# Kernel optimization log

Measured on AMD Instinct MI355X. Metric: run time of the kernel, lower is better.

The kernel has to match this reference:

```python
import jax, jax.numpy as jnp
import numpy as np
from jax import lax

H = 8          # num_heads
STATE = 16     # SSM state_dim
EPS = 1e-5


def layer_norm(x, g, b):
    mu = jnp.mean(x, axis=-1, keepdims=True)
    var = jnp.mean((x - mu) ** 2, axis=-1, keepdims=True)
    return (x - mu) / jnp.sqrt(var + EPS) * g + b


def linear(x, w, b):
    # torch nn.Linear convention: w [out,in]
    return x @ w.T + b


def cross_attn(q_in, kv_in, qw, qb, kw, kb, vw, vb, ow, ob, g, beta):
    B, Lq, D = q_in.shape
    Lk = kv_in.shape[1]
    hd = D // H
    Q = linear(q_in, qw, qb).reshape(B, Lq, H, hd).transpose(0, 2, 1, 3)
    K = linear(kv_in, kw, kb).reshape(B, Lk, H, hd).transpose(0, 2, 1, 3)
    V = linear(kv_in, vw, vb).reshape(B, Lk, H, hd).transpose(0, 2, 1, 3)
    scores = jnp.einsum('bhqd,bhkd->bhqk', Q, K) / (hd ** 0.5)
    w = jax.nn.softmax(scores, axis=-1)
    out = jnp.einsum('bhqk,bhkd->bhqd', w, V)
    out = out.transpose(0, 2, 1, 3).reshape(B, Lq, D)
    out = linear(out, ow, ob)
    out = layer_norm(out + q_in, g, beta)
    return out, w


def ssm(x, in_w, in_b, A, Bm, C, gw, gb, ow, ob):
    B, L, D = x.shape
    xp = linear(x, in_w, in_b)                      # [B,L,2D]
    x_in = xp[..., D:]                              # second chunk
    gate = jax.nn.sigmoid(linear(x, gw, gb))
    x_in = x_in * gate
    def step(h, xt):
        h = h @ A.T + xt @ Bm.T                     # [B,STATE]
        return h, h @ C.T                           # y [B,D]
    h0 = jnp.zeros((B, STATE), dtype=x.dtype)
    _, ys = lax.scan(step, h0, x_in.transpose(1, 0, 2))
    ys = ys.transpose(1, 0, 2)
    return linear(ys, ow, ob)


def mamba_block(x, p, i):
    y = ssm(layer_norm(x, p['m_ln1_g'][i], p['m_ln1_b'][i]),
            p['m_in_w'][i], p['m_in_b'][i], p['m_A'][i], p['m_B'][i], p['m_C'][i],
            p['m_gate_w'][i], p['m_gate_b'][i], p['m_sout_w'][i], p['m_sout_b'][i])
    x = x + y
    h = layer_norm(x, p['m_ln2_g'][i], p['m_ln2_b'][i])
    h = linear(h, p['m_f1_w'][i], p['m_f1_b'][i])
    h = jax.nn.gelu(h, approximate=False)
    h = linear(h, p['m_f2_w'][i], p['m_f2_b'][i])
    return x + h


def setup_inputs() -> dict:
    key = jax.random.key(0)
    ks = iter(jax.random.split(key, 64))
    B, L, D, BD, VD = 1024, 32, 256, 128, 256
    nB = 6
    def rn(shape, s=0.02):
        return jax.random.normal(next(ks), shape, dtype=jnp.float32) * s
    inp = {
        'ble_features': jax.random.normal(next(ks), (B, L, BD), dtype=jnp.float32),
        'visual_features': jax.random.normal(next(ks), (B, L, VD), dtype=jnp.float32),
        # modality projections
        'bp_w': rn((D, BD)), 'bp_b': jnp.zeros(D), 'bp_emb': rn((D,)),
        'bp_g': jnp.ones(D), 'bp_beta': jnp.zeros(D),
        'vp_w': rn((D, VD)), 'vp_b': jnp.zeros(D), 'vp_emb': rn((D,)),
        'vp_g': jnp.ones(D), 'vp_beta': jnp.zeros(D),
        # two cross-attentions stacked on axis 0: [0]=ble->vis, [1]=vis->ble
        'a_qw': rn((2, D, D)), 'a_qb': jnp.zeros((2, D)),
        'a_kw': rn((2, D, D)), 'a_kb': jnp.zeros((2, D)),
        'a_vw': rn((2, D, D)), 'a_vb': jnp.zeros((2, D)),
        'a_ow': rn((2, D, D)), 'a_ob': jnp.zeros((2, D)),
        'a_g': jnp.ones((2, D)), 'a_beta': jnp.zeros((2, D)),
        # 6 mamba blocks stacked on axis 0
        'm_ln1_g': jnp.ones((nB, D)), 'm_ln1_b': jnp.zeros((nB, D)),
        'm_in_w': rn((nB, 2 * D, D)), 'm_in_b': jnp.zeros((nB, 2 * D)),
        'm_A': rn((nB, STATE, STATE)), 'm_B': rn((nB, STATE, D)), 'm_C': rn((nB, D, STATE)),
        'm_gate_w': rn((nB, D, D)), 'm_gate_b': jnp.zeros((nB, D)),
        'm_sout_w': rn((nB, D, D)), 'm_sout_b': jnp.zeros((nB, D)),
        'm_ln2_g': jnp.ones((nB, D)), 'm_ln2_b': jnp.zeros((nB, D)),
        'm_f1_w': rn((nB, 4 * D, D)), 'm_f1_b': jnp.zeros((nB, 4 * D)),
        'm_f2_w': rn((nB, D, 4 * D)), 'm_f2_b': jnp.zeros((nB, D)),
        # final projection
        'fin_g': jnp.ones(D), 'fin_beta': jnp.zeros(D),
        'fin_w': rn((D, D)), 'fin_b': jnp.zeros(D),
    }
    return inp


def reference(ble_features, visual_features,
              bp_w, bp_b, bp_emb, bp_g, bp_beta,
              vp_w, vp_b, vp_emb, vp_g, vp_beta,
              a_qw, a_qb, a_kw, a_kb, a_vw, a_vb, a_ow, a_ob, a_g, a_beta,
              m_ln1_g, m_ln1_b, m_in_w, m_in_b, m_A, m_B, m_C,
              m_gate_w, m_gate_b, m_sout_w, m_sout_b,
              m_ln2_g, m_ln2_b, m_f1_w, m_f1_b, m_f2_w, m_f2_b,
              fin_g, fin_beta, fin_w, fin_b):
    ble = layer_norm(linear(ble_features, bp_w, bp_b) + bp_emb, bp_g, bp_beta)
    vis = layer_norm(linear(visual_features, vp_w, vp_b) + vp_emb, vp_g, vp_beta)
    # seq_len == target_length -> align_sequences is identity
    ble_att, w_b2v = cross_attn(ble, vis, a_qw[0], a_qb[0], a_kw[0], a_kb[0],
                                a_vw[0], a_vb[0], a_ow[0], a_ob[0], a_g[0], a_beta[0])
    vis_att, w_v2b = cross_attn(vis, ble, a_qw[1], a_qb[1], a_kw[1], a_kb[1],
                                a_vw[1], a_vb[1], a_ow[1], a_ob[1], a_g[1], a_beta[1])
    fused = ble_att + vis_att
    p = dict(m_ln1_g=m_ln1_g, m_ln1_b=m_ln1_b, m_in_w=m_in_w, m_in_b=m_in_b,
             m_A=m_A, m_B=m_B, m_C=m_C, m_gate_w=m_gate_w, m_gate_b=m_gate_b,
             m_sout_w=m_sout_w, m_sout_b=m_sout_b, m_ln2_g=m_ln2_g, m_ln2_b=m_ln2_b,
             m_f1_w=m_f1_w, m_f1_b=m_f1_b, m_f2_w=m_f2_w, m_f2_b=m_f2_b)
    for i in range(m_A.shape[0]):
        fused = mamba_block(fused, p, i)
    g = jnp.mean(fused, axis=1)
    g = layer_norm(g, fin_g, fin_beta)
    g = jax.nn.gelu(linear(g, fin_w, fin_b), approximate=False)
    wb = jnp.mean(w_b2v, axis=(1, 2, 3))
    wv = jnp.mean(w_v2b, axis=(1, 2, 3))
    tot = wb + wv + 1e-6
    return (g, wb / tot, wv / tot)
```

## Files before the change

### kernel.cpp

```cpp
#include <hip/hip_runtime.h>
#include <hip/hip_bf16.h>
#include <math.h>

static constexpr int Bsz  = 1024;
static constexpr int Lseq = 32;
static constexpr int Dm   = 256;
static constexpr int NROW = Bsz * Lseq;

typedef __attribute__((ext_vector_type(8))) short bf16x8;
typedef __attribute__((ext_vector_type(4))) float f32x4;

__device__ __forceinline__ float sigm_f(float x) {
    return 1.0f / (1.0f + __expf(-x));
}
__device__ __forceinline__ float gelu_f(float x) {
    const float u = x * (0.7978845608028654f + 0.0356774081f * x * x);
    return x * sigm_f(2.0f * u);
}
__device__ __forceinline__ float b2f(ushort u) {
    union { float f; uint v; } t; t.v = ((uint)u) << 16; return t.f;
}
__device__ __forceinline__ ushort f2b(float f) {
    union { float f; uint v; } t; t.f = f;
    const uint lsb = (t.v >> 16) & 1u;
    t.v += 0x7fffu + lsb;
    return (ushort)(t.v >> 16);
}

#define GLDS(gp, lp) __builtin_amdgcn_global_load_lds( \
    (const __attribute__((address_space(1))) void*)(gp), \
    (__attribute__((address_space(3))) void*)(lp), 16, 0, 0)


template<int ACT, bool OUTBF, int OMAP, int DUAL>
__global__ __launch_bounds__(256)
void mgemm(const ushort* __restrict__ X, const ushort* __restrict__ W,
           const ushort* __restrict__ W2,
           const float* __restrict__ b1, const float* __restrict__ b2,
           float* __restrict__ Cf, ushort* __restrict__ Cb,
           ushort* __restrict__ Cb2, int K, int M)
{
    __shared__ ushort As[8192];
    __shared__ ushort Bs[8192];
    __shared__ ushort Bs2[DUAL ? 8192 : 8];
    const int tid = threadIdx.x;
    const int w = tid >> 6, l = tid & 63;

    int f = blockIdx.y * gridDim.x + blockIdx.x;
    const int nwg = gridDim.x * gridDim.y;
    if ((nwg & 7) == 0) f = (f & 7) * (nwg >> 3) + (f >> 3);
    const int n0 = (f / gridDim.x) << 7;
    const int m0 = (f % gridDim.x) << 7;

    const int ric = l >> 3;
    const int sl  = l & 7;
    const ushort* gAp[4]; const ushort* gBp[4]; const ushort* gCp[DUAL ? 4 : 1];
    ushort* lAp[4]; ushort* lBp[4]; ushort* lCp[DUAL ? 4 : 1];
    #pragma unroll
    for (int c = 0; c < 4; ++c) {
        const int r = ((w << 2) + c) * 8 + ric;
        const int eo = (sl ^ (r & 7)) << 3;
        gAp[c] = X + (size_t)(n0 + r) * K + eo;
        gBp[c] = W + (size_t)(m0 + r) * K + eo;
        lAp[c] = As + (((w << 2) + c) << 9) ;
        lBp[c] = Bs + (((w << 2) + c) << 9);
        if constexpr (DUAL) {
            gCp[c] = W2 + (size_t)(m0 + r) * K + eo;
            lCp[c] = Bs2 + (((w << 2) + c) << 9);
        }
    }

    const int wr = (w >> 1) & 1, wc = w & 1;
    const int cl = l & 15, kg = l >> 4;
    int aoff[2][4], boff[2][4];
    #pragma unroll
    for (int sub = 0; sub < 2; ++sub) {
        const int s = sub * 4 + kg;
        #pragma unroll
        for (int m = 0; m < 4; ++m) {
            const int r = wr * 64 + m * 16 + cl;
            aoff[sub][m] = r * 64 + ((s ^ (r & 7)) << 3);
        }
        #pragma unroll
        for (int n = 0; n < 4; ++n) {
            const int r = wc * 64 + n * 16 + cl;
            boff[sub][n] = r * 64 + ((s ^ (r & 7)) << 3);
        }
    }

    f32x4 acc[4][4];
    f32x4 acc2[DUAL ? 4 : 1][DUAL ? 4 : 1];
    #pragma unroll
    for (int m = 0; m < 4; ++m)
        #pragma unroll
        for (int n = 0; n < 4; ++n) {
            acc[m][n] = (f32x4){0.f, 0.f, 0.f, 0.f};
            if constexpr (DUAL) acc2[m][n] = (f32x4){0.f, 0.f, 0.f, 0.f};
        }

    for (int kc = 0; kc < K; kc += 64) {
        #pragma unroll
        for (int c = 0; c < 4; ++c) {
            GLDS(gAp[c], lAp[c]); gAp[c] += 64;
            GLDS(gBp[c], lBp[c]); gBp[c] += 64;
            if constexpr (DUAL) { GLDS(gCp[c], lCp[c]); gCp[c] += 64; }
        }
        __syncthreads();
        #pragma unroll
        for (int sub = 0; sub < 2; ++sub) {
            bf16x8 av[4], bv[4];
            #pragma unroll
            for (int m = 0; m < 4; ++m) av[m] = *(const bf16x8*)(As + aoff[sub][m]);
            #pragma unroll
            for (int n = 0; n < 4; ++n) bv[n] = *(const bf16x8*)(Bs + boff[sub][n]);
            #pragma unroll
            for (int m = 0; m < 4; ++m)
                #pragma unroll
                for (int n = 0; n < 4; ++n)
                    acc[m][n] = __builtin_amdgcn_mfma_f32_16x16x32_bf16(
                        av[m], bv[n], acc[m][n], 0, 0, 0);
            if constexpr (DUAL) {
                bf16x8 cv[4];
                #pragma unroll
                for (int n = 0; n < 4; ++n) cv[n] = *(const bf16x8*)(Bs2 + boff[sub][n]);
                #pragma unroll
                for (int m = 0; m < 4; ++m)
                    #pragma unroll
                    for (int n = 0; n < 4; ++n)
                        acc2[m][n] = __builtin_amdgcn_mfma_f32_16x16x32_bf16(
                            av[m], cv[n], acc2[m][n], 0, 0, 0);
            }
        }
        __syncthreads();
    }

    const int colb = m0 + wc * 64 + cl;
    const int rowb = n0 + wr * 64 + (kg << 2);
    float biasA[4], biasB[4];
    #pragma unroll
    for (int n = 0; n < 4; ++n) {
        biasA[n] = (b1 != nullptr) ? b1[colb + n * 16] : 0.0f;
        if constexpr (DUAL) biasB[n] = b2[colb + n * 16];
    }

    if constexpr (OUTBF || DUAL != 0) {
        ushort* Rw = (w == 0) ? As : (w == 1) ? As + 4096
                   : (w == 2) ? Bs : Bs + 4096;
        const int rr = l >> 3, rc8 = (l & 7) << 3;
        const int nout = (DUAL == 2) ? 2 : 1;
        for (int which = 0; which < nout; ++which) {
            #pragma unroll
            for (int m = 0; m < 4; ++m)
                #pragma unroll
                for (int j = 0; j < 4; ++j) {
                    const int lrow = m * 16 + (kg << 2) + j;
                    #pragma unroll
                    for (int n = 0; n < 4; ++n) {
                        float v;
                        if (which == 0) {
                            v = acc[m][n][j] + biasA[n];
                            if constexpr (DUAL == 1)
                                v = sigm_f(v) * (acc2[m][n][j] + biasB[n]);
                            else if (ACT == 1) v = sigm_f(v);
                            else if (ACT == 2) v = gelu_f(v);
                        } else {
                            v = acc2[m][n][j] + biasB[n];
                        }
                        const int lcol = (n << 4) + cl;
                        Rw[lrow * 64 + (lcol ^ (((lrow >> 1) & 7) << 3))] = f2b(v);
                    }
                }
            ushort* dst = (which == 0) ? Cb : Cb2;
            #pragma unroll
            for (int p = 0; p < 8; ++p) {
                const int lrow = (p << 3) + rr;
                const bf16x8 v8 = *(const bf16x8*)(
                    Rw + lrow * 64 + (rc8 ^ (((lrow >> 1) & 7) << 3)));
                const size_t grow = (size_t)(n0 + wr * 64 + lrow);
                const int gcol = m0 + wc * 64 + rc8;
                size_t idx;
                if (OMAP == 1) idx = grow * 2048 + ((size_t)(gcol >> 4) << 6) + (gcol & 15);
                else           idx = grow * (size_t)M + gcol;
                *(bf16x8*)(dst + idx) = v8;
            }
        }
    } else {
        #pragma unroll
        for (int m = 0; m < 4; ++m)
            #pragma unroll
            for (int j = 0; j < 4; ++j) {
                const size_t row = (size_t)(rowb + m * 16 + j);
                #pragma unroll
                for (int n = 0; n < 4; ++n) {
                    float v = acc[m][n][j] + biasA[n];
                    if (ACT == 1) v = sigm_f(v);
                    else if (ACT == 2) v = gelu_f(v);
                    Cf[row * (size_t)M + colb + n * 16] = v;
                }
            }
    }
}

template<bool ADD_E, bool ACC_F, bool WRV, int LNOUT, bool HASB2>
__global__ __launch_bounds__(256)
void growln_k(const ushort* __restrict__ X, const ushort* __restrict__ W,
              const float* __restrict__ b1, const float* __restrict__ b2,
              const float* __restrict__ E, const float* __restrict__ g,
              const float* __restrict__ bt, float* __restrict__ Fres,
              ushort* __restrict__ Yb, int K)
{
    __shared__ ushort As[32 * 64];
    __shared__ ushort Bs[256 * 64];
    __shared__ float sred[32][2];
    __shared__ float qred[32][2];
    const int tid = threadIdx.x;
    const int w = tid >> 6, l = tid & 63;
    const int n0 = blockIdx.x << 5;
    const int rowg = w >> 1, colg = w & 1;

    const int ric = l >> 3, sl = l & 7;
    const ushort* gB[8]; ushort* lB[8];
    #pragma unroll
    for (int c = 0; c < 8; ++c) {
        const int rB = ((w << 3) + c) * 8 + ric;
        gB[c] = W + (size_t)rB * K + ((sl ^ (rB & 7)) << 3);
        lB[c] = Bs + (((w << 3) + c) << 9);
    }
    const int rA = (w << 3) + ric;
    const ushort* gA = X + (size_t)(n0 + rA) * K + ((sl ^ (rA & 7)) << 3);
    ushort* lA = As + (w << 9);

    const int cl = l & 15, kg = l >> 4;
    const int ar = rowg * 16 + cl;
    int aoff[2], boff[2][8];
    #pragma unroll
    for (int sub = 0; sub < 2; ++sub) {
        const int s = sub * 4 + kg;
        aoff[sub] = ar * 64 + ((s ^ (ar & 7)) << 3);
        #pragma unroll
        for (int n = 0; n < 8; ++n) {
            const int br = colg * 128 + n * 16 + cl;
            boff[sub][n] = br * 64 + ((s ^ (br & 7)) << 3);
        }
    }

    f32x4 acc[8];
    #pragma unroll
    for (int n = 0; n < 8; ++n) acc[n] = (f32x4){0.f, 0.f, 0.f, 0.f};

    for (int kc = 0; kc < K; kc += 64) {
        #pragma unroll
        for (int c = 0; c < 8; ++c) { GLDS(gB[c], lB[c]); gB[c] += 64; }
        GLDS(gA, lA); gA += 64;
        __syncthreads();
        #pragma unroll
        for (int sub = 0; sub < 2; ++sub) {
            const bf16x8 av = *(const bf16x8*)(As + aoff[sub]);
            #pragma unroll
            for (int n = 0; n < 8; ++n) {
                const bf16x8 bv = *(const bf16x8*)(Bs + boff[sub][n]);
                acc[n] = __builtin_amdgcn_mfma_f32_16x16x32_bf16(av, bv, acc[n], 0, 0, 0);
            }
        }
        __syncthreads();
    }

    float bA[8];
    #pragma unroll
    for (int n = 0; n < 8; ++n) {
        const int col = colg * 128 + n * 16 + cl;
        float v = (b1 != nullptr) ? b1[col] : 0.0f;
        if (HASB2) v += b2[col];
        bA[n] = v;
    }
    float gg[8], bb[8];
    if (LNOUT > 0) {
        #pragma unroll
        for (int n = 0; n < 8; ++n) {
            const int col = colg * 128 + n * 16 + cl;
            gg[n] = g[col]; bb[n] = bt[col];
        }
    }

    #pragma unroll
    for (int j = 0; j < 4; ++j) {
        const int lrow = rowg * 16 + (kg << 2) + j;
        const size_t rb = (size_t)(n0 + lrow) << 8;
        float s = 0.0f;
        #pragma unroll
        for (int n = 0; n < 8; ++n) {
            const size_t idx = rb + colg * 128 + n * 16 + cl;
            float x = acc[n][j] + bA[n];
            if (ADD_E) x += E[idx];
            if (ACC_F) x += Fres[idx];
            acc[n][j] = x; s += x;
        }
        if (WRV) {
            #pragma unroll
            for (int n = 0; n < 8; ++n)
                Fres[rb + colg * 128 + n * 16 + cl] = acc[n][j];
        }
        if (LNOUT > 0) {
            #pragma unroll
            for (int o = 1; o < 16; o <<= 1) s += __shfl_xor(s, o);
            if (cl == 0) sred[lrow][colg] = s;
        }
    }
    if (LNOUT > 0) {
        __syncthreads();
        float mu[4];
        #pragma unroll
        for (int j = 0; j < 4; ++j) {
            const int lrow = rowg * 16 + (kg << 2) + j;
            mu[j] = (sred[lrow][0] + sred[lrow][1]) * (1.0f / 256.0f);
            float q = 0.0f;
            #pragma unroll
            for (int n = 0; n < 8; ++n) { const float d = acc[n][j] - mu[j]; q += d * d; }
            #pragma unroll
            for (int o = 1; o < 16; o <<= 1) q += __shfl_xor(q, o);
            if (cl == 0) qred[lrow][colg] = q;
        }
        __syncthreads();
        #pragma unroll
        for (int j = 0; j < 4; ++j) {
            const int lrow = rowg * 16 + (kg << 2) + j;
            const size_t rb = (size_t)(n0 + lrow) << 8;
            const float rstd = rsqrtf((qred[lrow][0] + qred[lrow][1]) * (1.0f / 256.0f) + 1e-5f);
            #pragma unroll
            for (int n = 0; n < 8; ++n) {
                const float y = (acc[n][j] - mu[j]) * rstd * gg[n] + bb[n];
                const size_t idx = rb + colg * 128 + n * 16 + cl;
                if (LNOUT & 1) Yb[idx] = f2b(y);
                if (LNOUT == 2 || LNOUT == 3) Fres[idx] = y;
                if (LNOUT == 4) Fres[idx] += y;
            }
        }
    }
}

__global__ __launch_bounds__(256)
void ln_k(const float* __restrict__ X, const float* __restrict__ g,
          const float* __restrict__ bt, ushort* __restrict__ Yb)
{
    const int lane = threadIdx.x & 63;
    const int row  = (blockIdx.x << 2) + (threadIdx.x >> 6);
    const size_t base = (size_t)row * Dm + (lane << 2);
    float4 v = *reinterpret_cast<const float4*>(&X[base]);
    float s = v.x + v.y + v.z + v.w;
    #pragma unroll
    for (int o = 1; o < 64; o <<= 1) s += __shfl_xor(s, o);
    const float mu = s * (1.0f / 256.0f);
    const float d0 = v.x - mu, d1 = v.y - mu, d2 = v.z - mu, d3 = v.w - mu;
    float q = d0*d0 + d1*d1 + d2*d2 + d3*d3;
    #pragma unroll
    for (int o = 1; o < 64; o <<= 1) q += __shfl_xor(q, o);
    const float rstd = rsqrtf(q * (1.0f / 256.0f) + 1e-5f);
    const int c = lane << 2;
    const float4 gg = *reinterpret_cast<const float4*>(&g[c]);
    const float4 bb = *reinterpret_cast<const float4*>(&bt[c]);
    ushort4 ub;
    ub.x = f2b(d0*rstd*gg.x + bb.x); ub.y = f2b(d1*rstd*gg.y + bb.y);
    ub.z = f2b(d2*rstd*gg.z + bb.z); ub.w = f2b(d3*rstd*gg.w + bb.w);
    *reinterpret_cast<ushort4*>(&Yb[base]) = ub;
}

__global__ __launch_bounds__(256)
void attn_k(const ushort* __restrict__ Q, const ushort* __restrict__ K,
            const ushort* __restrict__ V, ushort* __restrict__ O)
{
    __shared__ float Qs[32][33], Ks[32][33], Vs[32][33], Ss[32][33];
    const int bh = blockIdx.x;
    const int b = bh >> 3, h = bh & 7;
    const int tid = threadIdx.x;
    const int r  = tid >> 3;
    const int c4 = (tid & 7) << 2;
    const size_t base = ((size_t)b * Lseq + r) * Dm + h * 32 + c4;
    {
        const ushort4 q = *reinterpret_cast<const ushort4*>(&Q[base]);
        Qs[r][c4+0]=b2f(q.x); Qs[r][c4+1]=b2f(q.y); Qs[r][c4+2]=b2f(q.z); Qs[r][c4+3]=b2f(q.w);
        const ushort4 k = *reinterpret_cast<const ushort4*>(&K[base]);
        Ks[r][c4+0]=b2f(k.x); Ks[r][c4+1]=b2f(k.y); Ks[r][c4+2]=b2f(k.z); Ks[r][c4+3]=b2f(k.w);
        const ushort4 v = *reinterpret_cast<const ushort4*>(&V[base]);
        Vs[r][c4+0]=b2f(v.x); Vs[r][c4+1]=b2f(v.y); Vs[r][c4+2]=b2f(v.z); Vs[r][c4+3]=b2f(v.w);
    }
    __syncthreads();
    float sc[4] = {0.f, 0.f, 0.f, 0.f};
    #pragma unroll
    for (int d = 0; d < 32; ++d) {
        const float qv = Qs[r][d];
        #pragma unroll
        for (int j = 0; j < 4; ++j) sc[j] = fmaf(qv, Ks[c4+j][d], sc[j]);
    }
    #pragma unroll
    for (int j = 0; j < 4; ++j) sc[j] *= 0.17677669529663687f;
    float mx = fmaxf(fmaxf(sc[0], sc[1]), fmaxf(sc[2], sc[3]));
    #pragma unroll
    for (int o = 1; o < 8; o <<= 1) mx = fmaxf(mx, __shfl_xor(mx, o));
    float sum = 0.f;
    #pragma unroll
    for (int j = 0; j < 4; ++j) { sc[j] = __expf(sc[j] - mx); sum += sc[j]; }
    #pragma unroll
    for (int o = 1; o < 8; o <<= 1) sum += __shfl_xor(sum, o);
    const float inv = 1.0f / sum;
    #pragma unroll
    for (int j = 0; j < 4; ++j) Ss[r][c4+j] = sc[j] * inv;
    __syncthreads();
    float o4[4] = {0.f, 0.f, 0.f, 0.f};
    #pragma unroll
    for (int k = 0; k < 32; ++k) {
        const float wv = Ss[r][k];
        #pragma unroll
        for (int j = 0; j < 4; ++j) o4[j] = fmaf(wv, Vs[k][c4+j], o4[j]);
    }
    ushort4 ob; ob.x=f2b(o4[0]); ob.y=f2b(o4[1]); ob.z=f2b(o4[2]); ob.w=f2b(o4[3]);
    *reinterpret_cast<ushort4*>(&O[base]) = ob;
}

__global__ __launch_bounds__(256)
void xb_gemm(const ushort* __restrict__ X, const ushort* __restrict__ Bw,
             ushort* __restrict__ XB)
{
    __shared__ ushort As[128 * 32];
    __shared__ ushort Bsf[16 * 256];
    const int tid = threadIdx.x;
    const int w = tid >> 6, l = tid & 63;
    const int n0 = blockIdx.x << 7;
    #pragma unroll
    for (int rep = 0; rep < 2; ++rep) {
        const int u = (rep << 8) + tid;
        const int r = u >> 5;
        const int c8 = (u & 31) << 3;
        const int di = (r * 256 + c8) ^ ((r & 7) << 3);
        *(bf16x8*)(Bsf + di) = *(const bf16x8*)(Bw + r * 256 + c8);
    }
    const int ric = l >> 2, slot = l & 3;
    const int rL0 = (w << 4) + ric, rL1 = rL0 + 64;
    const int sw0 = slot ^ ((rL0 >> 1) & 3), sw1 = slot ^ ((rL1 >> 1) & 3);
    const ushort* gA0 = X + (size_t)(n0 + rL0) * 256 + (sw0 << 3);
    const ushort* gA1 = X + (size_t)(n0 + rL1) * 256 + (sw1 << 3);
    ushort* lA0 = As + (w << 9);
    ushort* lA1 = As + ((w + 4) << 9);
    const int cl = l & 15, kg = l >> 4;
    int aoff[2];
    #pragma unroll
    for (int m = 0; m < 2; ++m) {
        const int r = w * 32 + m * 16 + cl;
        aoff[m] = r * 32 + ((kg ^ ((r >> 1) & 3)) << 3);
    }
    f32x4 acc[2] = {(f32x4){0.f,0.f,0.f,0.f}, (f32x4){0.f,0.f,0.f,0.f}};
    for (int kc = 0; kc < 256; kc += 32) {
        GLDS(gA0, lA0); GLDS(gA1, lA1);
        gA0 += 32; gA1 += 32;
        __syncthreads();
        const bf16x8 av0 = *(const bf16x8*)(As + aoff[0]);
        const bf16x8 av1 = *(const bf16x8*)(As + aoff[1]);
        const int bidx = (cl * 256 + kc + (kg << 3)) ^ ((cl & 7) << 3);
        const bf16x8 bv = *(const bf16x8*)(Bsf + bidx);
        acc[0] = __builtin_amdgcn_mfma_f32_16x16x32_bf16(av0, bv, acc[0], 0, 0, 0);
        acc[1] = __builtin_amdgcn_mfma_f32_16x16x32_bf16(av1, bv, acc[1], 0, 0, 0);
        __syncthreads();
    }
    #pragma unroll
    for (int m = 0; m < 2; ++m)
        #pragma unroll
        for (int j = 0; j < 4; ++j) {
            const int row = n0 + w * 32 + m * 16 + (kg << 2) + j;
            XB[(size_t)row * 16 + cl] = f2b(acc[m][j]);
        }
}

__global__ __launch_bounds__(256)
void powT_k(const float* __restrict__ A_all, ushort* __restrict__ T_all)
{
    __shared__ float P[2][16][16];
    __shared__ float Asm[16][16];
    const int layer = blockIdx.x;
    const float* A = A_all + layer * 256;
    ushort* T = T_all + (size_t)layer * 262144;
    const int tid = threadIdx.x;
    const int i = tid >> 4, j = tid & 15;
    Asm[i][j] = A[tid];
    const bf16x8 z = {0,0,0,0,0,0,0,0};
    for (int u = tid; u < 32768; u += 256)
        *(bf16x8*)(T + (size_t)u * 8) = z;
    P[0][i][j] = (i == j) ? 1.0f : 0.0f;
    __syncthreads();
    for (int k = 0; k < 32; ++k) {
        const float pv = P[k & 1][i][j];
        const ushort pb = f2b(pv);
        for (int tau = 0; tau + k < 32; ++tau)
            T[(size_t)((tau + k) * 16 + i) * 512 + tau * 16 + j] = pb;
        float acc = 0.0f;
        #pragma unroll
        for (int l2 = 0; l2 < 16; ++l2) acc = fmaf(P[k & 1][i][l2], Asm[l2][j], acc);
        P[(k & 1) ^ 1][i][j] = acc;
        __syncthreads();
    }
}

__global__ __launch_bounds__(256)
void zeroH_k(ushort* __restrict__ Hp)
{
    const int i = blockIdx.x * 256 + threadIdx.x;
    const bf16x8 z = {0,0,0,0,0,0,0,0};
    *(bf16x8*)(Hp + (size_t)i * 8) = z;
}

__global__ __launch_bounds__(256)
void wsc_k(const float* __restrict__ sw, const float* __restrict__ Cc,
           ushort* __restrict__ Wp)
{
    const int i = blockIdx.x >> 4;
    const int m = ((blockIdx.x & 15) << 4) + (threadIdx.x >> 4);
    const int s = threadIdx.x & 15;
    const float* swr = sw + ((size_t)i << 16) + (m << 8);
    const float* cc  = Cc + ((size_t)i << 12) + s;
    float acc = 0.0f;
    #pragma unroll 8
    for (int d = 0; d < 256; ++d) acc = fmaf(swr[d], cc[d << 4], acc);
    ushort* o = Wp + ((size_t)i << 14) + (m << 6);
    o[s] = f2b(acc);
    o[s + 16] = 0; o[s + 32] = 0; o[s + 48] = 0;
}

__global__ __launch_bounds__(256)
void meanL_k(const float* __restrict__ X, float* __restrict__ G)
{
    const int idx = blockIdx.x * 256 + threadIdx.x;
    const int b = idx >> 8, d = idx & 255;
    const float* xp = X + (size_t)b * (Lseq * Dm) + d;
    float s = 0.0f;
    #pragma unroll
    for (int t = 0; t < Lseq; ++t) s += xp[t << 8];
    G[idx] = s * (1.0f / 32.0f);
}

__global__ __launch_bounds__(256)
void fillw_k(float* __restrict__ out)
{
    const int i = blockIdx.x * 256 + threadIdx.x;
    const float wm = 1.0f / 32.0f;
    out[i] = wm / (wm + wm + 1e-6f);
}

__global__ __launch_bounds__(256)
void cast_k(const float* __restrict__ src, ushort* __restrict__ dst, int n4)
{
    const int i = blockIdx.x * 256 + threadIdx.x;
    if (i < n4) {
        const float4 v = reinterpret_cast<const float4*>(src)[i];
        ushort4 o; o.x = f2b(v.x); o.y = f2b(v.y); o.z = f2b(v.z); o.w = f2b(v.w);
        reinterpret_cast<ushort4*>(dst)[i] = o;
    }
}

__global__ __launch_bounds__(256)
void cast_inw_k(const float* __restrict__ src, ushort* __restrict__ dst)
{
    const int i = blockIdx.x * 256 + threadIdx.x;
    const int blk = i >> 14, rem = i & 16383;
    const float4 v = reinterpret_cast<const float4*>(
        src + (size_t)blk * 131072 + 65536)[rem];
    ushort4 o; o.x = f2b(v.x); o.y = f2b(v.y); o.z = f2b(v.z); o.w = f2b(v.w);
    reinterpret_cast<ushort4*>(dst)[i] = o;
}

extern "C" void kernel_launch(void* const* d_in, const int* in_sizes, int n_in,
                              void* d_out, int out_size, void* d_ws, size_t ws_size,
                              hipStream_t stream)
{
    const float* ble_f   = (const float*)d_in[0];
    const float* vis_f   = (const float*)d_in[1];
    const float* bp_w    = (const float*)d_in[2];
    const float* bp_b    = (const float*)d_in[3];
    const float* bp_emb  = (const float*)d_in[4];
    const float* bp_g    = (const float*)d_in[5];
    const float* bp_beta = (const float*)d_in[6];
    const float* vp_w    = (const float*)d_in[7];
    const float* vp_b    = (const float*)d_in[8];
    const float* vp_emb  = (const float*)d_in[9];
    const float* vp_g    = (const float*)d_in[10];
    const float* vp_beta = (const float*)d_in[11];
    const float* a_qw    = (const float*)d_in[12];
    const float* a_qb    = (const float*)d_in[13];
    const float* a_kw    = (const float*)d_in[14];
    const float* a_kb    = (const float*)d_in[15];
    const float* a_vw    = (const float*)d_in[16];
    const float* a_vb    = (const float*)d_in[17];
    const float* a_ow    = (const float*)d_in[18];
    const float* a_ob    = (const float*)d_in[19];
    const float* a_g     = (const float*)d_in[20];
    const float* a_beta  = (const float*)d_in[21];
    const float* m_ln1_g = (const float*)d_in[22];
    const float* m_ln1_b = (const float*)d_in[23];
    const float* m_in_w  = (const float*)d_in[24];
    const float* m_in_b  = (const float*)d_in[25];
    const float* m_A     = (const float*)d_in[26];
    const float* m_B     = (const float*)d_in[27];
    const float* m_C     = (const float*)d_in[28];
    const float* m_gw    = (const float*)d_in[29];
    const float* m_gb    = (const float*)d_in[30];
    const float* m_sw    = (const float*)d_in[31];
    const float* m_sb    = (const float*)d_in[32];
    const float* m_ln2_g = (const float*)d_in[33];
    const float* m_ln2_b = (const float*)d_in[34];
    const float* m_f1w   = (const float*)d_in[35];
    const float* m_f1b   = (const float*)d_in[36];
    const float* m_f2w   = (const float*)d_in[37];
    const float* m_f2b   = (const float*)d_in[38];
    const float* fin_g   = (const float*)d_in[39];
    const float* fin_beta= (const float*)d_in[40];
    const float* fin_w   = (const float*)d_in[41];
    const float* fin_b   = (const float*)d_in[42];

    float* out = (float*)d_out;
    float* ws  = (float*)d_ws;
    const size_t NDf = (size_t)NROW * Dm;

    float* F_res = ws;
    float* F0 = ws + 1 * NDf;
    float* F1 = ws + 2 * NDf;
    float* F2 = ws + 3 * NDf;
    ushort* S0 = (ushort*)(ws + 4 * NDf);
    ushort* S1 = S0 + NDf;
    ushort* S2 = S1 + NDf;
    ushort* S3 = S2 + NDf;
    ushort* S4 = S3 + NDf;
    ushort* Wa = S4 + NDf;
    ushort* W_bp  = Wa;
    ushort* W_vp  = W_bp + 32768;
    ushort* W_q   = W_vp + 65536;
    ushort* W_k   = W_q + 131072;
    ushort* W_v   = W_k + 131072;
    ushort* W_o   = W_v + 131072;
    ushort* W_g   = W_o + 131072;
    ushort* W_in  = W_g + 393216;
    ushort* W_f1  = W_in + 393216;
    ushort* W_f2  = W_f1 + 1572864;
    ushort* W_fin = W_f2 + 1572864;
    ushort* W_sc  = W_fin + 65536;
    ushort* Hpad  = W_sc + 98304;
    ushort* B_ble = (ushort*)F2;
    ushort* B_vis = B_ble + (size_t)NROW * 128;
    ushort* T_all = (ushort*)F2;
    ushort* W_bm  = T_all + 1572864;
    ushort* XBuf  = W_bm + 24576;

    const dim3 blk(256);
    auto cgrid = [](int n4) { return dim3((n4 + 255) / 256); };

    cast_k<<<cgrid(1048576), blk, 0, stream>>>(ble_f, B_ble, 1048576);
    cast_k<<<cgrid(2097152), blk, 0, stream>>>(vis_f, B_vis, 2097152);
    cast_k<<<cgrid(8192),   blk, 0, stream>>>(bp_w, W_bp, 8192);
    cast_k<<<cgrid(16384),  blk, 0, stream>>>(vp_w, W_vp, 16384);
    cast_k<<<cgrid(32768),  blk, 0, stream>>>(a_qw, W_q, 32768);
    cast_k<<<cgrid(32768),  blk, 0, stream>>>(a_kw, W_k, 32768);
    cast_k<<<cgrid(32768),  blk, 0, stream>>>(a_vw, W_v, 32768);
    cast_k<<<cgrid(32768),  blk, 0, stream>>>(a_ow, W_o, 32768);
    cast_k<<<cgrid(98304),  blk, 0, stream>>>(m_gw, W_g, 98304);
    cast_k<<<cgrid(393216), blk, 0, stream>>>(m_f1w, W_f1, 393216);
    cast_k<<<cgrid(393216), blk, 0, stream>>>(m_f2w, W_f2, 393216);
    cast_k<<<cgrid(16384),  blk, 0, stream>>>(fin_w, W_fin, 16384);
    cast_inw_k<<<cgrid(98304), blk, 0, stream>>>(m_in_w, W_in);
    wsc_k<<<96, blk, 0, stream>>>(m_sw, m_C, W_sc);

    auto gg = [](int M, int N) { return dim3(M / 128, N / 128); };
    const dim3 gRow(NROW / 32);

    growln_k<false,false,false,3,true><<<gRow, blk, 0, stream>>>(
        B_ble, W_bp, bp_b, bp_emb, nullptr, bp_g, bp_beta, F0, S0, 128);
    growln_k<false,false,false,3,true><<<gRow, blk, 0, stream>>>(
        B_vis, W_vp, vp_b, vp_emb, nullptr, vp_g, vp_beta, F1, S1, 256);

    for (int a = 0; a < 2; ++a) {
        const ushort* qin_b = (a == 0) ? S0 : S1;
        const ushort* kin_b = (a == 0) ? S1 : S0;
        const float*  qin_f = (a == 0) ? F0 : F1;
        const size_t wo = (size_t)a * 65536;
        const size_t bo = (size_t)a * 256;
        mgemm<0,true,0,0><<<gg(256, NROW), blk, 0, stream>>>(
            qin_b, W_q + wo, nullptr, a_qb + bo, nullptr, nullptr, S4, nullptr, 256, 256);
        mgemm<0,true,0,2><<<gg(256, NROW), blk, 0, stream>>>(
            kin_b, W_k + wo, W_v + wo, a_kb + bo, a_vb + bo, nullptr, S2, S3, 256, 256);
        attn_k<<<Bsz * 8, blk, 0, stream>>>(S4, S2, S3, S4);
        if (a == 0)
            growln_k<true,false,false,2,false><<<gRow, blk, 0, stream>>>(
                S4, W_o + wo, a_ob + bo, nullptr, qin_f, a_g + bo, a_beta + bo, F_res, nullptr, 256);
        else
            growln_k<true,false,false,4,false><<<gRow, blk, 0, stream>>>(
                S4, W_o + wo, a_ob + bo, nullptr, qin_f, a_g + bo, a_beta + bo, F_res, nullptr, 256);
    }

    powT_k<<<6, blk, 0, stream>>>(m_A, T_all);
    cast_k<<<cgrid(6144), blk, 0, stream>>>(m_B, W_bm, 6144);
    zeroH_k<<<1024, blk, 0, stream>>>(Hpad);

    ln_k<<<NROW/4, blk, 0, stream>>>(F_res, m_ln1_g, m_ln1_b, S0);

    for (int i = 0; i < 6; ++i) {
        mgemm<0,true,0,1><<<gg(256, NROW), blk, 0, stream>>>(
            S0, W_g + (size_t)i*65536, W_in + (size_t)i*65536,
            m_gb + i*256, m_in_b + (size_t)i*512 + 256, nullptr, S2, nullptr, 256, 256);
        xb_gemm<<<NROW/128, blk, 0, stream>>>(S2, W_bm + (size_t)i*4096, XBuf);
        mgemm<0,true,1,0><<<gg(512, 1024), blk, 0, stream>>>(
            XBuf, T_all + (size_t)i*262144, nullptr, nullptr, nullptr, nullptr, Hpad, nullptr, 512, 512);
        growln_k<false,true,true,1,false><<<gRow, blk, 0, stream>>>(
            Hpad, W_sc + (size_t)i*16384, m_sb + i*256, nullptr, nullptr,
            m_ln2_g + i*256, m_ln2_b + i*256, F_res, S0, 64);
        mgemm<2,true,0,0><<<gg(1024, NROW), blk, 0, stream>>>(
            S0, W_f1 + (size_t)i*262144, nullptr, m_f1b + i*1024, nullptr, nullptr, S1, nullptr, 256, 1024);
        if (i < 5)
            growln_k<false,true,true,1,false><<<gRow, blk, 0, stream>>>(
                S1, W_f2 + (size_t)i*262144, m_f2b + i*256, nullptr, nullptr,
                m_ln1_g + (i+1)*256, m_ln1_b + (i+1)*256, F_res, S0, 1024);
        else
            growln_k<false,true,true,0,false><<<gRow, blk, 0, stream>>>(
                S1, W_f2 + (size_t)i*262144, m_f2b + i*256, nullptr, nullptr,
                nullptr, nullptr, F_res, nullptr, 1024);
    }

    meanL_k<<<(Bsz * Dm) / 256, blk, 0, stream>>>(F_res, F0);
    ln_k<<<Bsz/4, blk, 0, stream>>>(F0, fin_g, fin_beta, S1);
    mgemm<2,false,0,0><<<gg(256, Bsz), blk, 0, stream>>>(
        S1, W_fin, nullptr, fin_b, nullptr, out, nullptr, nullptr, 256, 256);
    fillw_k<<<8, blk, 0, stream>>>(out + (size_t)Bsz * Dm);
}
```

Baseline: 1.165 ms.

## Double-buffer LDS tiles in single-output GEMMs and split the fused K/V GEMM

Non-dual mgemm and growln_k now double-buffer their LDS tiles. The next K-slice is issued via global_load_lds while MFMAs run on the current one, and wave priority is raised around the MFMA block. This drops one barrier per iteration and hides load latency. The fused K/V dual GEMM is replaced by two separate single-output GEMMs that use the pipelined path, which reads the activation twice but gives each kernel lower LDS and register pressure. LDS per block doubles, which may reduce occupancy. The single barrier per iteration may also leave a race between the next-tile prefetch and the previous reads.

```diff
diff --git a/kernel.cpp b/kernel.cpp
--- a/kernel.cpp
+++ b/kernel.cpp
@@ -40,8 +40,8 @@
            float* __restrict__ Cf, ushort* __restrict__ Cb,
            ushort* __restrict__ Cb2, int K, int M)
 {
-    __shared__ ushort As[8192];
-    __shared__ ushort Bs[8192];
+    __shared__ ushort As[DUAL ? 8192 : 16384];
+    __shared__ ushort Bs[DUAL ? 8192 : 16384];
     __shared__ ushort Bs2[DUAL ? 8192 : 8];
     const int tid = threadIdx.x;
     const int w = tid >> 6, l = tid & 63;
@@ -62,7 +62,7 @@
         const int eo = (sl ^ (r & 7)) << 3;
         gAp[c] = X + (size_t)(n0 + r) * K + eo;
         gBp[c] = W + (size_t)(m0 + r) * K + eo;
-        lAp[c] = As + (((w << 2) + c) << 9) ;
+        lAp[c] = As + (((w << 2) + c) << 9);
         lBp[c] = Bs + (((w << 2) + c) << 9);
         if constexpr (DUAL) {
             gCp[c] = W2 + (size_t)(m0 + r) * K + eo;
@@ -98,29 +98,28 @@
             if constexpr (DUAL) acc2[m][n] = (f32x4){0.f, 0.f, 0.f, 0.f};
         }
 
-    for (int kc = 0; kc < K; kc += 64) {
-        #pragma unroll
-        for (int c = 0; c < 4; ++c) {
-            GLDS(gAp[c], lAp[c]); gAp[c] += 64;
-            GLDS(gBp[c], lBp[c]); gBp[c] += 64;
-            if constexpr (DUAL) { GLDS(gCp[c], lCp[c]); gCp[c] += 64; }
-        }
-        __syncthreads();
-        #pragma unroll
-        for (int sub = 0; sub < 2; ++sub) {
-            bf16x8 av[4], bv[4];
-            #pragma unroll
-            for (int m = 0; m < 4; ++m) av[m] = *(const bf16x8*)(As + aoff[sub][m]);
-            #pragma unroll
-            for (int n = 0; n < 4; ++n) bv[n] = *(const bf16x8*)(Bs + boff[sub][n]);
-            #pragma unroll
-            for (int m = 0; m < 4; ++m)
-                #pragma unroll
-                for (int n = 0; n < 4; ++n)
-                    acc[m][n] = __builtin_amdgcn_mfma_f32_16x16x32_bf16(
-                        av[m], bv[n], acc[m][n], 0, 0, 0);
-            if constexpr (DUAL) {
-                bf16x8 cv[4];
+    if constexpr (DUAL != 0) {
+        for (int kc = 0; kc < K; kc += 64) {
+            #pragma unroll
+            for (int c = 0; c < 4; ++c) {
+                GLDS(gAp[c], lAp[c]); gAp[c] += 64;
+                GLDS(gBp[c], lBp[c]); gBp[c] += 64;
+                GLDS(gCp[c], lCp[c]); gCp[c] += 64;
+            }
+            __syncthreads();
+            #pragma unroll
+            for (int sub = 0; sub < 2; ++sub) {
+                bf16x8 av[4], bv[4], cv[4];
+                #pragma unroll
+                for (int m = 0; m < 4; ++m) av[m] = *(const bf16x8*)(As + aoff[sub][m]);
+                #pragma unroll
+                for (int n = 0; n < 4; ++n) bv[n] = *(const bf16x8*)(Bs + boff[sub][n]);
+                #pragma unroll
+                for (int m = 0; m < 4; ++m)
+                    #pragma unroll
+                    for (int n = 0; n < 4; ++n)
+                        acc[m][n] = __builtin_amdgcn_mfma_f32_16x16x32_bf16(
+                            av[m], bv[n], acc[m][n], 0, 0, 0);
                 #pragma unroll
                 for (int n = 0; n < 4; ++n) cv[n] = *(const bf16x8*)(Bs2 + boff[sub][n]);
                 #pragma unroll
@@ -130,8 +129,46 @@
                         acc2[m][n] = __builtin_amdgcn_mfma_f32_16x16x32_bf16(
                             av[m], cv[n], acc2[m][n], 0, 0, 0);
             }
+            __syncthreads();
+        }
+    } else {
+        const int nt = K >> 6;
+        #pragma unroll
+        for (int c = 0; c < 4; ++c) {
+            GLDS(gAp[c], lAp[c]); gAp[c] += 64;
+            GLDS(gBp[c], lBp[c]); gBp[c] += 64;
         }
         __syncthreads();
+        int cur = 0;
+        for (int t = 0; t < nt; ++t) {
+            if (t + 1 < nt) {
+                const int nb = (cur ^ 1) << 13;
+                #pragma unroll
+                for (int c = 0; c < 4; ++c) {
+                    GLDS(gAp[c], lAp[c] + nb); gAp[c] += 64;
+                    GLDS(gBp[c], lBp[c] + nb); gBp[c] += 64;
+                }
+            }
+            const int cb = cur << 13;
+            __builtin_amdgcn_s_setprio(1);
+            #pragma unroll
+            for (int sub = 0; sub < 2; ++sub) {
+                bf16x8 av[4], bv[4];
+                #pragma unroll
+                for (int m = 0; m < 4; ++m) av[m] = *(const bf16x8*)(As + cb + aoff[sub][m]);
+                #pragma unroll
+                for (int n = 0; n < 4; ++n) bv[n] = *(const bf16x8*)(Bs + cb + boff[sub][n]);
+                #pragma unroll
+                for (int m = 0; m < 4; ++m)
+                    #pragma unroll
+                    for (int n = 0; n < 4; ++n)
+                        acc[m][n] = __builtin_amdgcn_mfma_f32_16x16x32_bf16(
+                            av[m], bv[n], acc[m][n], 0, 0, 0);
+            }
+            __builtin_amdgcn_s_setprio(0);
+            __syncthreads();
+            cur ^= 1;
+        }
     }
 
     const int colb = m0 + wc * 64 + cl;
@@ -144,8 +181,9 @@
     }
 
     if constexpr (OUTBF || DUAL != 0) {
-        ushort* Rw = (w == 0) ? As : (w == 1) ? As + 4096
-                   : (w == 2) ? Bs : Bs + 4096;
+        ushort* Rw;
+        if constexpr (DUAL) Rw = (w < 2) ? As + (w << 12) : Bs + ((w - 2) << 12);
+        else                Rw = As + (w << 12);
         const int rr = l >> 3, rc8 = (l & 7) << 3;
         const int nout = (DUAL == 2) ? 2 : 1;
         for (int which = 0; which < nout; ++which) {
@@ -209,8 +247,8 @@
               const float* __restrict__ bt, float* __restrict__ Fres,
               ushort* __restrict__ Yb, int K)
 {
-    __shared__ ushort As[32 * 64];
-    __shared__ ushort Bs[256 * 64];
+    __shared__ ushort As[2 * 2048];
+    __shared__ ushort Bs[2 * 16384];
     __shared__ float sred[32][2];
     __shared__ float qred[32][2];
     const int tid = threadIdx.x;
@@ -248,21 +286,34 @@
     #pragma unroll
     for (int n = 0; n < 8; ++n) acc[n] = (f32x4){0.f, 0.f, 0.f, 0.f};
 
-    for (int kc = 0; kc < K; kc += 64) {
-        #pragma unroll
-        for (int c = 0; c < 8; ++c) { GLDS(gB[c], lB[c]); gB[c] += 64; }
-        GLDS(gA, lA); gA += 64;
-        __syncthreads();
+    const int nt = K >> 6;
+    #pragma unroll
+    for (int c = 0; c < 8; ++c) { GLDS(gB[c], lB[c]); gB[c] += 64; }
+    GLDS(gA, lA); gA += 64;
+    __syncthreads();
+    int cur = 0;
+    for (int t = 0; t < nt; ++t) {
+        if (t + 1 < nt) {
+            const int nbB = (cur ^ 1) << 14;
+            const int nbA = (cur ^ 1) << 11;
+            #pragma unroll
+            for (int c = 0; c < 8; ++c) { GLDS(gB[c], lB[c] + nbB); gB[c] += 64; }
+            GLDS(gA, lA + nbA); gA += 64;
+        }
+        const int cbB = cur << 14, cbA = cur << 11;
+        __builtin_amdgcn_s_setprio(1);
         #pragma unroll
         for (int sub = 0; sub < 2; ++sub) {
-            const bf16x8 av = *(const bf16x8*)(As + aoff[sub]);
+            const bf16x8 av = *(const bf16x8*)(As + cbA + aoff[sub]);
             #pragma unroll
             for (int n = 0; n < 8; ++n) {
-                const bf16x8 bv = *(const bf16x8*)(Bs + boff[sub][n]);
+                const bf16x8 bv = *(const bf16x8*)(Bs + cbB + boff[sub][n]);
                 acc[n] = __builtin_amdgcn_mfma_f32_16x16x32_bf16(av, bv, acc[n], 0, 0, 0);
             }
         }
+        __builtin_amdgcn_s_setprio(0);
         __syncthreads();
+        cur ^= 1;
     }
 
     float bA[8];
@@ -680,8 +731,10 @@
         const size_t bo = (size_t)a * 256;
         mgemm<0,true,0,0><<<gg(256, NROW), blk, 0, stream>>>(
             qin_b, W_q + wo, nullptr, a_qb + bo, nullptr, nullptr, S4, nullptr, 256, 256);
-        mgemm<0,true,0,2><<<gg(256, NROW), blk, 0, stream>>>(
-            kin_b, W_k + wo, W_v + wo, a_kb + bo, a_vb + bo, nullptr, S2, S3, 256, 256);
+        mgemm<0,true,0,0><<<gg(256, NROW), blk, 0, stream>>>(
+            kin_b, W_k + wo, nullptr, a_kb + bo, nullptr, nullptr, S2, nullptr, 256, 256);
+        mgemm<0,true,0,0><<<gg(256, NROW), blk, 0, stream>>>(
+            kin_b, W_v + wo, nullptr, a_vb + bo, nullptr, nullptr, S3, nullptr, 256, 256);
         attn_k<<<Bsz * 8, blk, 0, stream>>>(S4, S2, S3, S4);
         if (a == 0)
             growln_k<true,false,false,2,false><<<gRow, blk, 0, stream>>>(
```

Measured after the change: 1.245 ms. 1.07x slower.
